# Kernel optimization log

Hardware: AMD Instinct MI355X
Metric: run time of the kernel (lower is better)

## Reference

```python
import jax, jax.numpy as jnp
import numpy as np

# Static module configuration (matches init_kwargs)
B, CIN, COUT, K, H, W = 4, 32, 32, 3, 128, 128
UM = 2                      # um_dim: 2D vector fields
NW = ((K - 1) // 2) * 4     # num_weights = radius*4 = 4


def setup_inputs() -> dict:
    key = jax.random.key(0)
    k1, k2, k3 = jax.random.split(key, 3)
    params = jax.random.normal(k1, (COUT, CIN, NW, 4), jnp.float32)
    basis = jax.random.normal(k2, (NW, 4, K, K, UM, UM), jnp.float32)
    # Replicate the init-time scaling of the torch module:
    # std over the (non-zero) outer-product kernel, then scale params and basis.
    init_kernel = jnp.einsum('abcd,cdefgh->abcdefgh', params, basis)
    stds = jnp.std(init_kernel)  # random basis -> all entries nonzero
    scaler = jnp.sqrt(0.6 / (np.sqrt(CIN) * (K ** 2) * stds))
    params = params * scaler
    basis = basis * scaler
    bias_term = jnp.ones((1, COUT, 2, 1, 1), jnp.float32) / 100.0
    b = jnp.float32(0.01)
    xx = jax.random.normal(k3, (B, CIN * UM, H, W), jnp.float32)
    return {'xx': xx, 'params': params, 'basis': basis,
            'bias_term': bias_term, 'b': b}


def _forward(xx, params, basis, bias_term, b):
    Bn, C, Hh, Ww = xx.shape
    I, O = CIN, COUT
    # --- get_kernel: einsum + transposes -> conv weight (O*2, I*2, K, K) ---
    Kr = jnp.einsum('abcd,cdefgh->abefgh', params, basis)      # (O,I,K,K,2,2)
    kernel = jnp.transpose(Kr, (0, 4, 1, 5, 2, 3)).reshape(O * 2, I * 2, K, K)
    # --- unfold with replicate padding: P[b,c,kh,kw,h,w] ---
    xp = jnp.pad(xx, ((0, 0), (0, 0), (1, 1), (1, 1)), mode='edge')
    P = jnp.stack([xp[:, :, i:i + Hh, j:j + Ww]
                   for i in range(K) for j in range(K)], axis=2)
    P = P.reshape(Bn, C, K, K, Hh, Ww)
    # --- per-window mean subtraction over (input_channels, kh, kw) ---
    P5 = P.reshape(Bn, I, UM, K, K, Hh, Ww)
    avgs = P5.mean(axis=(1, 3, 4), keepdims=True)              # (B,1,2,1,1,H,W)
    P = (P5 - avgs).reshape(Bn, C, K, K, Hh, Ww)
    avgs = avgs[:, :, :, 0, 0]                                 # (B,1,2,H,W)
    # --- strided conv2d on the blown-up grid == this einsum:
    # big[b,c,3h+di,3w+dj] = P[b,c,kh=dj,kw=di,h,w], so kernel (di,dj)=(p,q)
    # pairs with patch (kh=q, kw=p).
    out = jnp.einsum('bcqphw,ocpq->bohw', P, kernel)           # (B,O*2,H,W)
    out = out.reshape(Bn, O, 2, Hh, Ww) + bias_term
    # --- 'relu' vector activation: normalize, zero where norm <= b ---
    norm = jnp.sqrt(out[:, :, 0] ** 2 + out[:, :, 1] ** 2)[:, :, None]
    out = jnp.where(norm - b <= 0.0, 0.0, out / norm)
    # --- add_mean ---
    out = out + avgs
    return out.reshape(Bn, O * 2, Hh, Ww)


def reference(xx, params, basis, bias_term, b):
    return _forward(xx, params, basis, bias_term, b)
```

## Files before the change

### kernel.cpp

```cpp
#include <hip/hip_runtime.h>

#define BN 4
#define CH 64
#define HH 128
#define WW 128
#define PIX (HH*WW)

#define OFF_WL  0
#define OFF_S   36864
#define OFF_CS  36992
#define OFF_AVG 168064

__global__ void k_weights(const float* __restrict__ params,
                          const float* __restrict__ basis,
                          float* __restrict__ Wl) {
    int idx = blockIdx.x * blockDim.x + threadIdx.x;
    if (idx >= 64 * 9 * 64) return;
    int oc  = idx & 63;
    int tap = (idx >> 6) % 9;
    int c   = idx / (64 * 9);
    int q = tap / 3, p = tap % 3;
    int o = oc >> 1, g = oc & 1;
    int i = c >> 1, u = c & 1;
    float s = 0.f;
    #pragma unroll
    for (int n = 0; n < 4; ++n)
        #pragma unroll
        for (int d = 0; d < 4; ++d)
            s = fmaf(params[((o * 32 + i) * 4 + n) * 4 + d],
                     basis[((((n * 4 + d) * 3 + p) * 3 + q) * 2 + g) * 2 + u], s);
    Wl[idx] = s;
}

__global__ void k_ssum(const float* __restrict__ Wl, float* __restrict__ S) {
    int t = threadIdx.x;
    if (t >= 128) return;
    int u = t >> 6, oc = t & 63;
    float s = 0.f;
    for (int i = 0; i < 32; ++i)
        for (int tap = 0; tap < 9; ++tap)
            s += Wl[((i * 2 + u) * 9 + tap) * 64 + oc];
    S[t] = s;
}

__global__ void k_colsum(const float* __restrict__ x, float* __restrict__ cs) {
    int idx = blockIdx.x * blockDim.x + threadIdx.x;
    if (idx >= BN * 2 * PIX) return;
    int pix = idx & (PIX - 1);
    int u   = (idx >> 14) & 1;
    int b   = idx >> 15;
    const float* xb = x + b * CH * PIX + u * PIX + pix;
    float s = 0.f;
    #pragma unroll
    for (int i = 0; i < 32; ++i) s += xb[i * 2 * PIX];
    cs[idx] = s;
}

__global__ void k_avg(const float* __restrict__ cs, float* __restrict__ avg) {
    int idx = blockIdx.x * blockDim.x + threadIdx.x;
    if (idx >= BN * 2 * PIX) return;
    int w  = idx & (WW - 1);
    int h  = (idx >> 7) & (HH - 1);
    int bu = idx >> 14;
    const float* c0 = cs + bu * PIX;
    int hm = h > 0 ? h - 1 : 0, hp = h < HH - 1 ? h + 1 : HH - 1;
    int wm = w > 0 ? w - 1 : 0, wp = w < WW - 1 ? w + 1 : WW - 1;
    float s = c0[hm * WW + wm] + c0[hm * WW + w] + c0[hm * WW + wp]
            + c0[h  * WW + wm] + c0[h  * WW + w] + c0[h  * WW + wp]
            + c0[hp * WW + wm] + c0[hp * WW + w] + c0[hp * WW + wp];
    avg[idx] = s * (1.0f / 288.0f);
}

__global__ __launch_bounds__(256) void k_main(
    const float* __restrict__ x,
    const float* __restrict__ Wl,
    const float* __restrict__ S,
    const float* __restrict__ bias,
    const float* __restrict__ avg,
    const float* __restrict__ bptr,
    float* __restrict__ out)
{
    int tile   = blockIdx.x;
    int ocbase = blockIdx.y * 16;
    int b      = blockIdx.z;
    int ty = threadIdx.x >> 4, tx = threadIdx.x & 15;
    int h = (tile >> 3) * 16 + ty;
    int w = (tile & 7) * 16 + tx;

    int hm = h > 0 ? h - 1 : 0, hp = h < HH - 1 ? h + 1 : HH - 1;
    int wm = w > 0 ? w - 1 : 0, wp = w < WW - 1 ? w + 1 : WW - 1;
    int rowoff[3] = { hm * WW, h * WW, hp * WW };
    int coloff[3] = { wm, w, wp };

    float acc[16];
    #pragma unroll
    for (int j = 0; j < 16; ++j) acc[j] = 0.f;

    const float* xc = x + b * CH * PIX;
    const float* wc = Wl + ocbase;
    for (int c = 0; c < CH; ++c) {
        float xv[9];
        #pragma unroll
        for (int q = 0; q < 3; ++q)
            #pragma unroll
            for (int p = 0; p < 3; ++p)
                xv[q * 3 + p] = xc[rowoff[q] + coloff[p]];
        #pragma unroll
        for (int t = 0; t < 9; ++t) {
            #pragma unroll
            for (int j = 0; j < 16; ++j)
                acc[j] = fmaf(xv[t], wc[t * 64 + j], acc[j]);
        }
        xc += PIX;
        wc += 9 * 64;
    }

    int pix = h * WW + w;
    float a0 = avg[(b * 2 + 0) * PIX + pix];
    float a1 = avg[(b * 2 + 1) * PIX + pix];
    float bthr = bptr[0];

    float t[16];
    #pragma unroll
    for (int j = 0; j < 16; ++j) {
        int oc = ocbase + j;
        t[j] = acc[j] - a0 * S[oc] - a1 * S[64 + oc] + bias[oc];
    }

    float* ob = out + b * CH * PIX + pix;
    #pragma unroll
    for (int j = 0; j < 16; j += 2) {
        float n = sqrtf(t[j] * t[j] + t[j + 1] * t[j + 1]);
        float r0, r1;
        if (n - bthr <= 0.f) { r0 = 0.f; r1 = 0.f; }
        else { r0 = t[j] / n; r1 = t[j + 1] / n; }
        ob[(ocbase + j)     * PIX] = r0 + a0;
        ob[(ocbase + j + 1) * PIX] = r1 + a1;
    }
}

extern "C" void kernel_launch(void* const* d_in, const int* in_sizes, int n_in,
                              void* d_out, int out_size, void* d_ws, size_t ws_size,
                              hipStream_t stream) {
    const float* xx     = (const float*)d_in[0];
    const float* params = (const float*)d_in[1];
    const float* basis  = (const float*)d_in[2];
    const float* bias   = (const float*)d_in[3];
    const float* bptr   = (const float*)d_in[4];
    float* out = (float*)d_out;
    float* ws  = (float*)d_ws;

    float* Wl  = ws + OFF_WL;
    float* S   = ws + OFF_S;
    float* cs  = ws + OFF_CS;
    float* avg = ws + OFF_AVG;

    k_weights<<<(64 * 9 * 64 + 255) / 256, 256, 0, stream>>>(params, basis, Wl);
    k_ssum<<<1, 128, 0, stream>>>(Wl, S);
    k_colsum<<<(BN * 2 * PIX + 255) / 256, 256, 0, stream>>>(xx, cs);
    k_avg<<<(BN * 2 * PIX + 255) / 256, 256, 0, stream>>>(cs, avg);

    dim3 grid(64, 4, BN);
    k_main<<<grid, 256, 0, stream>>>(xx, Wl, S, bias, avg, bptr, out);
}
```

Measured before the change: 146.3 us.

## Fuse prep kernels into one launch and split main conv over more output blocks

Merges the weight build, weight-sum, column-sum and 3x3 average kernels into a single block-dispatched prep kernel. S is now computed directly from params and basis, and the averages use a shared-memory halo tile, which drops three launches and the cs intermediate. The main conv kernel now computes 8 output channels per block instead of 16, doubling the grid and setting a launch-bounds occupancy hint. It also prefetches the next channel's 9 inputs in registers. Halving the channels per block doubles the input loads per output and adds register pressure from the prefetch buffer.

```diff
diff --git a/kernel.cpp b/kernel.cpp
--- a/kernel.cpp
+++ b/kernel.cpp
@@ -8,70 +8,86 @@
 
 #define OFF_WL  0
 #define OFF_S   36864
-#define OFF_CS  36992
-#define OFF_AVG 168064
+#define OFF_AVG 36992
 
-__global__ void k_weights(const float* __restrict__ params,
-                          const float* __restrict__ basis,
-                          float* __restrict__ Wl) {
-    int idx = blockIdx.x * blockDim.x + threadIdx.x;
-    if (idx >= 64 * 9 * 64) return;
-    int oc  = idx & 63;
-    int tap = (idx >> 6) % 9;
-    int c   = idx / (64 * 9);
-    int q = tap / 3, p = tap % 3;
-    int o = oc >> 1, g = oc & 1;
-    int i = c >> 1, u = c & 1;
-    float s = 0.f;
-    #pragma unroll
-    for (int n = 0; n < 4; ++n)
-        #pragma unroll
-        for (int d = 0; d < 4; ++d)
-            s = fmaf(params[((o * 32 + i) * 4 + n) * 4 + d],
-                     basis[((((n * 4 + d) * 3 + p) * 3 + q) * 2 + g) * 2 + u], s);
-    Wl[idx] = s;
+__device__ __forceinline__ int iclamp(int v, int lo, int hi) {
+    return v < lo ? lo : (v > hi ? hi : v);
 }
 
-__global__ void k_ssum(const float* __restrict__ Wl, float* __restrict__ S) {
-    int t = threadIdx.x;
-    if (t >= 128) return;
-    int u = t >> 6, oc = t & 63;
-    float s = 0.f;
-    for (int i = 0; i < 32; ++i)
-        for (int tap = 0; tap < 9; ++tap)
-            s += Wl[((i * 2 + u) * 9 + tap) * 64 + oc];
-    S[t] = s;
+__global__ __launch_bounds__(256) void k_prep(const float* __restrict__ params,
+                                              const float* __restrict__ basis,
+                                              const float* __restrict__ x,
+                                              float* __restrict__ Wl,
+                                              float* __restrict__ S,
+                                              float* __restrict__ avg) {
+    int bx = blockIdx.x;
+    if (bx < 144) {
+        int idx = bx * 256 + threadIdx.x;
+        int oc  = idx & 63;
+        int tap = (idx >> 6) % 9;
+        int c   = idx / 576;
+        int q = tap / 3, p = tap % 3;
+        int o = oc >> 1, g = oc & 1;
+        int i = c >> 1, u = c & 1;
+        float s = 0.f;
+        #pragma unroll
+        for (int n = 0; n < 4; ++n)
+            #pragma unroll
+            for (int d = 0; d < 4; ++d)
+                s = fmaf(params[((o * 32 + i) * 4 + n) * 4 + d],
+                         basis[((((n * 4 + d) * 3 + p) * 3 + q) * 2 + g) * 2 + u], s);
+        Wl[idx] = s;
+    } else if (bx == 144) {
+        int t = threadIdx.x;
+        if (t < 128) {
+            int u = t >> 6, oc = t & 63;
+            int o = oc >> 1, g = oc & 1;
+            float s = 0.f;
+            #pragma unroll
+            for (int nd = 0; nd < 16; ++nd) {
+                int n = nd >> 2, d = nd & 3;
+                float pa = 0.f;
+                for (int i = 0; i < 32; ++i)
+                    pa += params[((o * 32 + i) * 4 + n) * 4 + d];
+                float sb = 0.f;
+                #pragma unroll
+                for (int e = 0; e < 3; ++e)
+                    #pragma unroll
+                    for (int f = 0; f < 3; ++f)
+                        sb += basis[((((n * 4 + d) * 3 + e) * 3 + f) * 2 + g) * 2 + u];
+                s = fmaf(pa, sb, s);
+            }
+            S[t] = s;
+        }
+    } else {
+        int id = bx - 145;
+        int tile = id & 63;
+        int u    = (id >> 6) & 1;
+        int b    = id >> 7;
+        int ty0 = (tile >> 3) * 16, tx0 = (tile & 7) * 16;
+
+        __shared__ float hs[18][19];
+        int t = threadIdx.x;
+        for (int cell = t; cell < 324; cell += 256) {
+            int hy = cell / 18, hx = cell - (cell / 18) * 18;
+            int gy = iclamp(ty0 + hy - 1, 0, HH - 1);
+            int gx = iclamp(tx0 + hx - 1, 0, WW - 1);
+            const float* xp = x + ((size_t)b * CH + u) * PIX + gy * WW + gx;
+            float s = 0.f;
+            #pragma unroll
+            for (int i = 0; i < 32; ++i) s += xp[(size_t)i * 2 * PIX];
+            hs[hy][hx] = s;
+        }
+        __syncthreads();
+        int py = t >> 4, px = t & 15;
+        float s = hs[py][px]     + hs[py][px + 1]     + hs[py][px + 2]
+                + hs[py + 1][px] + hs[py + 1][px + 1] + hs[py + 1][px + 2]
+                + hs[py + 2][px] + hs[py + 2][px + 1] + hs[py + 2][px + 2];
+        avg[(size_t)(b * 2 + u) * PIX + (ty0 + py) * WW + (tx0 + px)] = s * (1.0f / 288.0f);
+    }
 }
 
-__global__ void k_colsum(const float* __restrict__ x, float* __restrict__ cs) {
-    int idx = blockIdx.x * blockDim.x + threadIdx.x;
-    if (idx >= BN * 2 * PIX) return;
-    int pix = idx & (PIX - 1);
-    int u   = (idx >> 14) & 1;
-    int b   = idx >> 15;
-    const float* xb = x + b * CH * PIX + u * PIX + pix;
-    float s = 0.f;
-    #pragma unroll
-    for (int i = 0; i < 32; ++i) s += xb[i * 2 * PIX];
-    cs[idx] = s;
-}
-
-__global__ void k_avg(const float* __restrict__ cs, float* __restrict__ avg) {
-    int idx = blockIdx.x * blockDim.x + threadIdx.x;
-    if (idx >= BN * 2 * PIX) return;
-    int w  = idx & (WW - 1);
-    int h  = (idx >> 7) & (HH - 1);
-    int bu = idx >> 14;
-    const float* c0 = cs + bu * PIX;
-    int hm = h > 0 ? h - 1 : 0, hp = h < HH - 1 ? h + 1 : HH - 1;
-    int wm = w > 0 ? w - 1 : 0, wp = w < WW - 1 ? w + 1 : WW - 1;
-    float s = c0[hm * WW + wm] + c0[hm * WW + w] + c0[hm * WW + wp]
-            + c0[h  * WW + wm] + c0[h  * WW + w] + c0[h  * WW + wp]
-            + c0[hp * WW + wm] + c0[hp * WW + w] + c0[hp * WW + wp];
-    avg[idx] = s * (1.0f / 288.0f);
-}
-
-__global__ __launch_bounds__(256) void k_main(
+__global__ __launch_bounds__(256, 8) void k_main(
     const float* __restrict__ x,
     const float* __restrict__ Wl,
     const float* __restrict__ S,
@@ -81,7 +97,7 @@
     float* __restrict__ out)
 {
     int tile   = blockIdx.x;
-    int ocbase = blockIdx.y * 16;
+    int ocbase = blockIdx.y * 8;
     int b      = blockIdx.z;
     int ty = threadIdx.x >> 4, tx = threadIdx.x & 15;
     int h = (tile >> 3) * 16 + ty;
@@ -91,51 +107,61 @@
     int wm = w > 0 ? w - 1 : 0, wp = w < WW - 1 ? w + 1 : WW - 1;
     int rowoff[3] = { hm * WW, h * WW, hp * WW };
     int coloff[3] = { wm, w, wp };
+    int off[9];
+    #pragma unroll
+    for (int r = 0; r < 3; ++r)
+        #pragma unroll
+        for (int p = 0; p < 3; ++p)
+            off[r * 3 + p] = rowoff[r] + coloff[p];
 
-    float acc[16];
+    float acc[8];
     #pragma unroll
-    for (int j = 0; j < 16; ++j) acc[j] = 0.f;
+    for (int j = 0; j < 8; ++j) acc[j] = 0.f;
 
-    const float* xc = x + b * CH * PIX;
+    const float* xc = x + (size_t)b * CH * PIX;
     const float* wc = Wl + ocbase;
+
+    float xv[9];
+    #pragma unroll
+    for (int k = 0; k < 9; ++k) xv[k] = xc[off[k]];
+
     for (int c = 0; c < CH; ++c) {
-        float xv[9];
+        const float* xn = xc + (c < CH - 1 ? PIX : 0);
+        float xf[9];
         #pragma unroll
-        for (int q = 0; q < 3; ++q)
-            #pragma unroll
-            for (int p = 0; p < 3; ++p)
-                xv[q * 3 + p] = xc[rowoff[q] + coloff[p]];
+        for (int k = 0; k < 9; ++k) xf[k] = xn[off[k]];
+
         #pragma unroll
         for (int t = 0; t < 9; ++t) {
+            const float* wt = wc + t * 64;
+            float xt = xv[t];
             #pragma unroll
-            for (int j = 0; j < 16; ++j)
-                acc[j] = fmaf(xv[t], wc[t * 64 + j], acc[j]);
+            for (int j = 0; j < 8; ++j)
+                acc[j] = fmaf(xt, wt[j], acc[j]);
         }
+        #pragma unroll
+        for (int k = 0; k < 9; ++k) xv[k] = xf[k];
         xc += PIX;
-        wc += 9 * 64;
+        wc += 576;
     }
 
     int pix = h * WW + w;
-    float a0 = avg[(b * 2 + 0) * PIX + pix];
-    float a1 = avg[(b * 2 + 1) * PIX + pix];
+    float a0 = avg[(size_t)(b * 2 + 0) * PIX + pix];
+    float a1 = avg[(size_t)(b * 2 + 1) * PIX + pix];
     float bthr = bptr[0];
 
-    float t[16];
+    float* ob = out + (size_t)b * CH * PIX + pix;
     #pragma unroll
-    for (int j = 0; j < 16; ++j) {
+    for (int j = 0; j < 8; j += 2) {
         int oc = ocbase + j;
-        t[j] = acc[j] - a0 * S[oc] - a1 * S[64 + oc] + bias[oc];
-    }
-
-    float* ob = out + b * CH * PIX + pix;
-    #pragma unroll
-    for (int j = 0; j < 16; j += 2) {
-        float n = sqrtf(t[j] * t[j] + t[j + 1] * t[j + 1]);
+        float t0 = acc[j]     - a0 * S[oc]     - a1 * S[64 + oc]     + bias[oc];
+        float t1 = acc[j + 1] - a0 * S[oc + 1] - a1 * S[64 + oc + 1] + bias[oc + 1];
+        float n = sqrtf(t0 * t0 + t1 * t1);
         float r0, r1;
         if (n - bthr <= 0.f) { r0 = 0.f; r1 = 0.f; }
-        else { r0 = t[j] / n; r1 = t[j + 1] / n; }
-        ob[(ocbase + j)     * PIX] = r0 + a0;
-        ob[(ocbase + j + 1) * PIX] = r1 + a1;
+        else { r0 = t0 / n; r1 = t1 / n; }
+        ob[(size_t)oc * PIX]       = r0 + a0;
+        ob[(size_t)(oc + 1) * PIX] = r1 + a1;
     }
 }
 
@@ -152,14 +178,10 @@
 
     float* Wl  = ws + OFF_WL;
     float* S   = ws + OFF_S;
-    float* cs  = ws + OFF_CS;
     float* avg = ws + OFF_AVG;
 
-    k_weights<<<(64 * 9 * 64 + 255) / 256, 256, 0, stream>>>(params, basis, Wl);
-    k_ssum<<<1, 128, 0, stream>>>(Wl, S);
-    k_colsum<<<(BN * 2 * PIX + 255) / 256, 256, 0, stream>>>(xx, cs);
-    k_avg<<<(BN * 2 * PIX + 255) / 256, 256, 0, stream>>>(cs, avg);
+    k_prep<<<657, 256, 0, stream>>>(params, basis, xx, Wl, S, avg);
 
-    dim3 grid(64, 4, BN);
+    dim3 grid(64, 8, BN);
     k_main<<<grid, 256, 0, stream>>>(xx, Wl, S, bias, avg, bptr, out);
 }
```

Result: slower. 171.1 us (+17.0%).
